# Kernel optimization log

Measured on AMD Instinct MI355X. Metric: run time of the kernel, lower is better.

The kernel has to match this reference:

```python
import jax, jax.numpy as jnp
import numpy as np

N_NODES = 20000
N_EDGES = 320000
D = 256          # out_channels (== in_channels here, so PyG zero-padding is a no-op)
NUM_LAYERS = 5


def setup_inputs() -> dict:
    key = jax.random.key(0)
    ks = jax.random.split(key, 8)
    x = jax.random.normal(ks[0], (N_NODES, D), dtype=jnp.float32)
    src = jax.random.randint(ks[1], (N_EDGES,), 0, N_NODES)
    dst = jax.random.randint(ks[2], (N_EDGES,), 0, N_NODES)
    edge_index = jnp.stack([src, dst]).astype(jnp.int64)
    edge_attr = jax.random.uniform(ks[3], (N_EDGES,), dtype=jnp.float32)
    s = 1.0 / np.sqrt(D)
    # per-layer message transform weights [L, D, D]
    weight = jax.random.uniform(ks[4], (NUM_LAYERS, D, D), minval=-s, maxval=s, dtype=jnp.float32)
    # GRUCell parameters (torch layout: [3*D, D] for W_ih/W_hh, [3*D] biases; gate order r, z, n)
    w_ih = jax.random.uniform(ks[5], (3 * D, D), minval=-s, maxval=s, dtype=jnp.float32)
    w_hh = jax.random.uniform(ks[6], (3 * D, D), minval=-s, maxval=s, dtype=jnp.float32)
    b = jax.random.uniform(ks[7], (2, 3 * D), minval=-s, maxval=s, dtype=jnp.float32)
    return {"x": x, "edge_index": edge_index, "edge_attr": edge_attr,
            "weight": weight, "w_ih": w_ih, "w_hh": w_hh,
            "b_ih": b[0], "b_hh": b[1]}


def gru_cell(m, h, w_ih, w_hh, b_ih, b_hh):
    gi = m @ w_ih.T + b_ih   # [N, 3D]
    gh = h @ w_hh.T + b_hh   # [N, 3D]
    i_r, i_z, i_n = jnp.split(gi, 3, axis=1)
    h_r, h_z, h_n = jnp.split(gh, 3, axis=1)
    r = jax.nn.sigmoid(i_r + h_r)
    z = jax.nn.sigmoid(i_z + h_z)
    n = jnp.tanh(i_n + r * h_n)
    return (1.0 - z) * n + z * h


def reference(x, edge_index, edge_attr, weight, w_ih, w_hh, b_ih, b_hh):
    src = edge_index[0]
    dst = edge_index[1]
    n_nodes = x.shape[0]
    h = x  # in_channels == out_channels, so no zero padding needed
    for i in range(weight.shape[0]):
        m = h @ weight[i]                                  # [N, D] transformed messages
        msgs = m[src] * edge_attr[:, None]                 # gather + edge weighting [E, D]
        agg = jax.ops.segment_sum(msgs, dst, num_segments=n_nodes)  # scatter-add [N, D]
        h = gru_cell(agg, h, w_ih, w_hh, b_ih, b_hh)
    return h
```

## Files before the change

### kernel.cpp

```cpp
#include <hip/hip_runtime.h>
#include <hip/hip_bf16.h>

#define NN 20000
#define NE 320000
#define DD 256

typedef __attribute__((ext_vector_type(8))) short bf16x8;
typedef __attribute__((ext_vector_type(4))) float f32x4;
typedef __attribute__((ext_vector_type(4))) int   int4v;
typedef __attribute__((ext_vector_type(4))) float float4v;

typedef __attribute__((address_space(1))) unsigned int gas_uint;
typedef __attribute__((address_space(3))) unsigned int las_uint;
static __device__ __forceinline__ void gload16(const void* g, void* l) {
    __builtin_amdgcn_global_load_lds((gas_uint*)g, (las_uint*)l, 16, 0, 0);
}

__device__ __forceinline__ unsigned short f2bf(float f) {
    union { float f; unsigned u; } v; v.f = f;
    unsigned r = v.u + 0x7fffu + ((v.u >> 16) & 1u);
    return (unsigned short)(r >> 16);
}
__device__ __forceinline__ float bf2f(unsigned short h) {
    union { unsigned u; float f; } v; v.u = ((unsigned)h) << 16;
    return v.f;
}
__device__ __forceinline__ float fast_sigmoid(float x) {
    return 1.f / (1.f + __expf(-x));
}
__device__ __forceinline__ float fast_tanh(float x) {
    x = fminf(fmaxf(x, -30.f), 30.f);
    float e = __expf(-2.f * x);
    return (1.f - e) / (1.f + e);
}

__global__ void prep_kernel(const float* __restrict__ x, unsigned short* __restrict__ hbfA,
                            const float* __restrict__ W, unsigned short* __restrict__ wnb,
                            const float* __restrict__ wih, unsigned short* __restrict__ wihb,
                            const float* __restrict__ whh, unsigned short* __restrict__ wc5,
                            const int* __restrict__ edst, int* __restrict__ deg) {
    const int b = blockIdx.x, t = threadIdx.x;
    if (b < 5000) {
        int i = (b * 256 + t) * 4;
        float4v v = *reinterpret_cast<const float4v*>(x + i);
        uint2 o;
        o.x = (unsigned)f2bf(v.x) | ((unsigned)f2bf(v.y) << 16);
        o.y = (unsigned)f2bf(v.z) | ((unsigned)f2bf(v.w) << 16);
        *reinterpret_cast<uint2*>(hbfA + i) = o;
    } else if (b < 5320) {
        int i = ((b - 5000) * 256 + t) * 4;
        float4v v = *reinterpret_cast<const float4v*>(W + i);
        uint2 o;
        o.x = (unsigned)f2bf(v.x) | ((unsigned)f2bf(v.y) << 16);
        o.y = (unsigned)f2bf(v.z) | ((unsigned)f2bf(v.w) << 16);
        *reinterpret_cast<uint2*>(wnb + i) = o;
    } else if (b < 5512) {
        int i = ((b - 5320) * 256 + t) * 4;
        float4v v = *reinterpret_cast<const float4v*>(wih + i);
        uint2 o;
        o.x = (unsigned)f2bf(v.x) | ((unsigned)f2bf(v.y) << 16);
        o.y = (unsigned)f2bf(v.z) | ((unsigned)f2bf(v.w) << 16);
        *reinterpret_cast<uint2*>(wihb + i) = o;
    } else if (b < 5704) {
        int id = (b - 5512) * 256 + t;
        int n3 = id >> 6, k0 = (id & 63) * 4;
        int g3 = (n3 >> 4) % 3;
        int d = (n3 / 48) * 16 + (n3 & 15);
        int gr = g3 * 256 + d;
        float4v v = *reinterpret_cast<const float4v*>(whh + gr * 256 + k0);
        uint2 o;
        o.x = (unsigned)f2bf(v.x) | ((unsigned)f2bf(v.y) << 16);
        o.y = (unsigned)f2bf(v.z) | ((unsigned)f2bf(v.w) << 16);
#pragma unroll
        for (int l = 0; l < 5; ++l)
            *reinterpret_cast<uint2*>(wc5 + ((size_t)(l * 2 + 1) * 768 + n3) * 256 + k0) = o;
    } else {
        int e = (b - 5704) * 256 + t;
        if (e < NE) atomicAdd(&deg[edst[e]], 1);
    }
}

__global__ __launch_bounds__(256) void pgemm_kernel(const unsigned short* __restrict__ A,
                                                    const unsigned short* __restrict__ Bt,
                                                    unsigned short* __restrict__ wc5) {
    __shared__ __align__(16) unsigned short As[128 * 64];
    __shared__ __align__(16) unsigned short Bs[64 * 64];
    const int t = threadIdx.x;
    const int lane = t & 63;
    const int w = t >> 6;
    const int wr = w >> 1, wc = w & 1;
    const int m0 = blockIdx.y * 128;
    const int n0 = blockIdx.x * 64;

    f32x4 acc[4][2];
    const f32x4 z4 = {0.f, 0.f, 0.f, 0.f};
    for (int i = 0; i < 4; ++i) for (int j = 0; j < 2; ++j) acc[i][j] = z4;

    for (int kt = 0; kt < 4; ++kt) {
        const int k0 = kt * 64;
#pragma unroll
        for (int rnd = 0; rnd < 4; ++rnd) {
            int cb = rnd * 256 + (w << 6);
            int c = cb + lane;
            int row = c >> 3, sl = c & 7;
            int gsl = sl ^ (row & 7);
            gload16(A + (size_t)(m0 + row) * 256 + k0 + gsl * 8, &As[cb * 8]);
        }
#pragma unroll
        for (int rnd = 0; rnd < 2; ++rnd) {
            int cb = rnd * 256 + (w << 6);
            int c = cb + lane;
            int row = c >> 3, sl = c & 7;
            int gsl = sl ^ (row & 7);
            gload16(Bt + (size_t)(n0 + row) * 256 + k0 + gsl * 8, &Bs[cb * 8]);
        }
        __syncthreads();
#pragma unroll
        for (int ks = 0; ks < 2; ++ks) {
            const int slot = ks * 4 + (lane >> 4);
            bf16x8 a[4], b[2];
#pragma unroll
            for (int mi = 0; mi < 4; ++mi) {
                int row = wr * 64 + mi * 16 + (lane & 15);
                a[mi] = *reinterpret_cast<const bf16x8*>(&As[row * 64 + ((slot ^ (row & 7)) << 3)]);
            }
#pragma unroll
            for (int ni = 0; ni < 2; ++ni) {
                int row = wc * 32 + ni * 16 + (lane & 15);
                b[ni] = *reinterpret_cast<const bf16x8*>(&Bs[row * 64 + ((slot ^ (row & 7)) << 3)]);
            }
#pragma unroll
            for (int mi = 0; mi < 4; ++mi)
#pragma unroll
                for (int ni = 0; ni < 2; ++ni)
                    acc[mi][ni] = __builtin_amdgcn_mfma_f32_16x16x32_bf16(a[mi], b[ni], acc[mi][ni], 0, 0, 0);
        }
        __syncthreads();
    }
#pragma unroll
    for (int mi = 0; mi < 4; ++mi)
#pragma unroll
        for (int ni = 0; ni < 2; ++ni)
#pragma unroll
            for (int r = 0; r < 4; ++r) {
                int grow = m0 + wr * 64 + mi * 16 + (lane >> 4) * 4 + r;
                int gcol = n0 + wc * 32 + ni * 16 + (lane & 15);
                int l = grow >> 8, k = grow & 255;
                int g3 = gcol >> 8, d = gcol & 255;
                int n3 = (d >> 4) * 48 + g3 * 16 + (d & 15);
                wc5[((size_t)(l * 2) * 768 + n3) * 256 + k] = f2bf(acc[mi][ni][r]);
            }
}


__global__ __launch_bounds__(1024) void scan_kernel(const int* __restrict__ deg, int* __restrict__ base) {
    __shared__ int part[1024];
    const int t = threadIdx.x;
    const int CH = 20;
    int start = t * CH;
    int s = 0;
    for (int i = 0; i < CH; ++i) { int idx = start + i; if (idx < NN) s += deg[idx]; }
    part[t] = s; __syncthreads();
    for (int off = 1; off < 1024; off <<= 1) {
        int v = (t >= off) ? part[t - off] : 0;
        __syncthreads();
        part[t] += v;
        __syncthreads();
    }
    int run = (t == 0) ? 0 : part[t - 1];
    for (int i = 0; i < CH; ++i) {
        int idx = start + i;
        if (idx < NN) { base[idx] = run; run += deg[idx]; }
    }
    if (t == 1023) base[NN] = run;
}

__global__ void fill_kernel(const int* __restrict__ src, const int* __restrict__ dst,
                            const float* __restrict__ attr, const int* __restrict__ base,
                            int* __restrict__ cursor, int* __restrict__ ssrc,
                            float* __restrict__ sattr) {
    int e = blockIdx.x * 256 + threadIdx.x;
    if (e >= NE) return;
    int d = dst[e];
    int pos = base[d] + atomicAdd(&cursor[d], 1);
    ssrc[pos] = src[e];
    sattr[pos] = attr[e];
}

__global__ __launch_bounds__(256) void gather_agg_kernel(const unsigned short* __restrict__ Hbf,
                                                         const int* __restrict__ base,
                                                         const int* __restrict__ ssrc,
                                                         const float* __restrict__ sattr,
                                                         unsigned short* __restrict__ AggBf) {
    int node = blockIdx.x * 4 + (threadIdx.x >> 6);
    if (node >= NN) return;
    int lane = threadIdx.x & 63;
    int q = lane >> 4;
    int ql = lane & 15;
    int b0 = base[node], b1 = base[node + 1];
    float ac[16];
#pragma unroll
    for (int j = 0; j < 16; ++j) ac[j] = 0.f;
    for (int p = b0 + q; p < b1; p += 4) {
        int s = ssrc[p];
        float a = sattr[p];
        const unsigned short* rowp = Hbf + (size_t)s * 256 + ql * 16;
        int4v v0 = *reinterpret_cast<const int4v*>(rowp);
        int4v v1 = *reinterpret_cast<const int4v*>(rowp + 8);
#pragma unroll
        for (int j = 0; j < 4; ++j) {
            unsigned u0 = (unsigned)v0[j];
            ac[2 * j]     += a * bf2f((unsigned short)(u0 & 0xffff));
            ac[2 * j + 1] += a * bf2f((unsigned short)(u0 >> 16));
            unsigned u1 = (unsigned)v1[j];
            ac[8 + 2 * j]     += a * bf2f((unsigned short)(u1 & 0xffff));
            ac[8 + 2 * j + 1] += a * bf2f((unsigned short)(u1 >> 16));
        }
    }
#pragma unroll
    for (int j = 0; j < 16; ++j) {
        ac[j] += __shfl_xor(ac[j], 16);
        ac[j] += __shfl_xor(ac[j], 32);
    }
    if (q == 0) {
        unsigned ou[8];
#pragma unroll
        for (int j = 0; j < 8; ++j)
            ou[j] = (unsigned)f2bf(ac[2 * j]) | ((unsigned)f2bf(ac[2 * j + 1]) << 16);
        unsigned short* op = AggBf + (size_t)node * 256 + ql * 16;
        *reinterpret_cast<int4v*>(op)     = *reinterpret_cast<int4v*>(&ou[0]);
        *reinterpret_cast<int4v*>(op + 8) = *reinterpret_cast<int4v*>(&ou[4]);
    }
}

__global__ __launch_bounds__(512) void gru4_kernel(const unsigned short* __restrict__ Abf,
                                                   const unsigned short* __restrict__ Hbf,
                                                   const unsigned short* __restrict__ Wc,
                                                   const float* __restrict__ b_ih,
                                                   const float* __restrict__ b_hh,
                                                   const float* __restrict__ x_f32,
                                                   float* __restrict__ h_out,
                                                   unsigned short* __restrict__ Hbf_out,
                                                   int first, int last) {
    __shared__ __align__(16) unsigned short As[128 * 64];
    __shared__ __align__(16) unsigned short Bs[96 * 64];
    const int t = threadIdx.x;
    const int lane = t & 63;
    const int w = t >> 6;
    const int wm = w >> 1, wn = w & 1;
    int b = blockIdx.x;
    int ww = (b & 7) * 158 + (b >> 3);
    const int mt = ww >> 3, dgp = ww & 7;
    const int m0 = mt * 128;

    f32x4 aR[2], aZ[2], aI[2], aH[2];
    const f32x4 z4 = {0.f, 0.f, 0.f, 0.f};
#pragma unroll
    for (int i = 0; i < 2; ++i) { aR[i] = z4; aZ[i] = z4; aI[i] = z4; aH[i] = z4; }

    auto do_half = [&](const unsigned short* __restrict__ aptr,
                       const unsigned short* __restrict__ wcb,
                       f32x4 (&aX)[2]) {
        for (int kq = 0; kq < 4; ++kq) {
            const int ka = kq * 64;
#pragma unroll
            for (int rnd = 0; rnd < 2; ++rnd) {
                int cb = rnd * 512 + (w << 6);
                int c = cb + lane;
                int row = c >> 3, sl = c & 7;
                int gsl = sl ^ (row & 7);
                gload16(aptr + (size_t)(m0 + row) * 256 + ka + gsl * 8, &As[cb * 8]);
            }
            {
                int cb = (w << 6);
                int c = cb + lane;
                int row = c >> 3, sl = c & 7;
                int gsl = sl ^ (row & 7);
                gload16(wcb + (size_t)(dgp * 96 + row) * 256 + ka + gsl * 8, &Bs[cb * 8]);
            }
            if (w < 4) {
                int cb = 512 + (w << 6);
                int c = cb + lane;
                int row = c >> 3, sl = c & 7;
                int gsl = sl ^ (row & 7);
                gload16(wcb + (size_t)(dgp * 96 + row) * 256 + ka + gsl * 8, &Bs[cb * 8]);
            }
            __syncthreads();
#pragma unroll
            for (int ks = 0; ks < 2; ++ks) {
                const int slot = ks * 4 + (lane >> 4);
                bf16x8 a[2], bfr[3];
#pragma unroll
                for (int mi = 0; mi < 2; ++mi) {
                    int row = wm * 32 + mi * 16 + (lane & 15);
                    a[mi] = *reinterpret_cast<const bf16x8*>(&As[row * 64 + ((slot ^ (row & 7)) << 3)]);
                }
#pragma unroll
                for (int g3 = 0; g3 < 3; ++g3) {
                    int row = wn * 48 + g3 * 16 + (lane & 15);
                    bfr[g3] = *reinterpret_cast<const bf16x8*>(&Bs[row * 64 + ((slot ^ (row & 7)) << 3)]);
                }
#pragma unroll
                for (int mi = 0; mi < 2; ++mi) {
                    aR[mi] = __builtin_amdgcn_mfma_f32_16x16x32_bf16(a[mi], bfr[0], aR[mi], 0, 0, 0);
                    aZ[mi] = __builtin_amdgcn_mfma_f32_16x16x32_bf16(a[mi], bfr[1], aZ[mi], 0, 0, 0);
                    aX[mi] = __builtin_amdgcn_mfma_f32_16x16x32_bf16(a[mi], bfr[2], aX[mi], 0, 0, 0);
                }
            }
            __syncthreads();
        }
    };

    do_half(Abf, Wc, aI);
    do_half(Hbf, Wc + 768 * 256, aH);

    const int d = (dgp * 2 + wn) * 16 + (lane & 15);
    const float bir = b_ih[d],        bhr = b_hh[d];
    const float biz = b_ih[256 + d],  bhz = b_hh[256 + d];
    const float bin_ = b_ih[512 + d], bhn = b_hh[512 + d];
#pragma unroll
    for (int mi = 0; mi < 2; ++mi)
#pragma unroll
        for (int r = 0; r < 4; ++r) {
            int grow = m0 + wm * 32 + mi * 16 + (lane >> 4) * 4 + r;
            if (grow >= NN) continue;
            size_t idx = (size_t)grow * 256 + d;
            float rr = fast_sigmoid(aR[mi][r] + bir + bhr);
            float zz = fast_sigmoid(aZ[mi][r] + biz + bhz);
            float nn = fast_tanh(aI[mi][r] + bin_ + rr * (aH[mi][r] + bhn));
            float hp = first ? x_f32[idx] : bf2f(Hbf[idx]);
            float hv = (1.f - zz) * nn + zz * hp;
            if (last) h_out[idx] = hv;
            Hbf_out[idx] = f2bf(hv);
        }
}


extern "C" void kernel_launch(void* const* d_in, const int* in_sizes, int n_in,
                              void* d_out, int out_size, void* d_ws, size_t ws_size,
                              hipStream_t stream) {
    const float* x     = (const float*)d_in[0];
    const int*   eidx  = (const int*)d_in[1];
    const float* eattr = (const float*)d_in[2];
    const float* W     = (const float*)d_in[3];
    const float* wih   = (const float*)d_in[4];
    const float* whh   = (const float*)d_in[5];
    const float* bih   = (const float*)d_in[6];
    const float* bhh   = (const float*)d_in[7];
    float* out = (float*)d_out;
    const int* esrc = eidx;
    const int* edst = eidx + NE;

    char* p = (char*)d_ws;
    auto alloc = [&](size_t bytes) -> char* {
        char* r = p; p += (bytes + 255) & ~(size_t)255; return r;
    };
    unsigned short* hbfA  = (unsigned short*)alloc((size_t)NN * DD * 2);
    unsigned short* hbfB  = (unsigned short*)alloc((size_t)NN * DD * 2);
    unsigned short* aggbf = (unsigned short*)alloc((size_t)NN * DD * 2);
    unsigned short* wnb   = (unsigned short*)alloc((size_t)5 * DD * DD * 2);
    unsigned short* wihb  = (unsigned short*)alloc((size_t)768 * DD * 2);
    unsigned short* wc5   = (unsigned short*)alloc((size_t)5 * 2 * 768 * 256 * 2);
    int*   degcur = (int*)alloc((size_t)2 * NN * 4);
    int*   deg    = degcur;
    int*   cursor = degcur + NN;
    int*   basep  = (int*)alloc((size_t)(NN + 1) * 4);
    int*   ssrc   = (int*)alloc((size_t)NE * 4);
    float* sattr  = (float*)alloc((size_t)NE * 4);
    alloc(262144);

    hipMemsetAsync(degcur, 0, (size_t)2 * NN * 4, stream);
    prep_kernel<<<6954, 256, 0, stream>>>(x, hbfA, W, wnb, wih, wihb, whh, wc5, edst, deg);
    pgemm_kernel<<<dim3(12, 10), 256, 0, stream>>>(wnb, wihb, wc5);
    scan_kernel<<<1, 1024, 0, stream>>>(deg, basep);
    fill_kernel<<<1250, 256, 0, stream>>>(esrc, edst, eattr, basep, cursor, ssrc, sattr);

    unsigned short* hb_cur = hbfA;
    unsigned short* hb_nxt = hbfB;
    for (int l = 0; l < 5; ++l) {
        gather_agg_kernel<<<5000, 256, 0, stream>>>(hb_cur, basep, ssrc, sattr, aggbf);
        gru4_kernel<<<1264, 512, 0, stream>>>(aggbf, hb_cur, wc5 + (size_t)l * 2 * 768 * 256,
                                              bih, bhh, x, out, hb_nxt,
                                              (l == 0) ? 1 : 0, (l == 4) ? 1 : 0);
        unsigned short* tmp = hb_cur; hb_cur = hb_nxt; hb_nxt = tmp;
    }
    (void)in_sizes; (void)n_in; (void)out_size; (void)ws_size;
}
```

Measured before the change: 343.8 us.

## Fuse all layers into one cooperative persistent kernel with grid syncs

Replaces the ten per-layer gather and GRU launches with a single cooperative persistent kernel that loops over layers and separates the aggregation and GRU phases with grid-wide syncs. It also drops the separate cursor array by atomically bumping the scan base directly in fill, then recovers each segment start as end minus degree. The goal is to remove launch gaps and tail effects between the many short kernels. The costs are a persistent grid capped by occupancy (launch bounds 512 threads, 8 blocks), grid-sync overhead, and host-side attribute and occupancy queries on every call.

```diff
diff --git a/kernel.cpp b/kernel.cpp
--- a/kernel.cpp
+++ b/kernel.cpp
@@ -1,5 +1,8 @@
 #include <hip/hip_runtime.h>
 #include <hip/hip_bf16.h>
+#include <hip/hip_cooperative_groups.h>
+
+namespace cg = cooperative_groups;
 
 #define NN 20000
 #define NE 320000
@@ -176,19 +179,19 @@
 }
 
 __global__ void fill_kernel(const int* __restrict__ src, const int* __restrict__ dst,
-                            const float* __restrict__ attr, const int* __restrict__ base,
-                            int* __restrict__ cursor, int* __restrict__ ssrc,
-                            float* __restrict__ sattr) {
+                            const float* __restrict__ attr, int* __restrict__ base,
+                            int* __restrict__ ssrc, float* __restrict__ sattr) {
     int e = blockIdx.x * 256 + threadIdx.x;
     if (e >= NE) return;
     int d = dst[e];
-    int pos = base[d] + atomicAdd(&cursor[d], 1);
+    int pos = atomicAdd(&base[d], 1);
     ssrc[pos] = src[e];
     sattr[pos] = attr[e];
 }
 
 __global__ __launch_bounds__(256) void gather_agg_kernel(const unsigned short* __restrict__ Hbf,
-                                                         const int* __restrict__ base,
+                                                         const int* __restrict__ basee,
+                                                         const int* __restrict__ deg,
                                                          const int* __restrict__ ssrc,
                                                          const float* __restrict__ sattr,
                                                          unsigned short* __restrict__ AggBf) {
@@ -197,7 +200,8 @@
     int lane = threadIdx.x & 63;
     int q = lane >> 4;
     int ql = lane & 15;
-    int b0 = base[node], b1 = base[node + 1];
+    int b1 = basee[node];
+    int b0 = b1 - deg[node];
     float ac[16];
 #pragma unroll
     for (int j = 0; j < 16; ++j) ac[j] = 0.f;
@@ -335,6 +339,160 @@
         }
 }
 
+__global__ __launch_bounds__(512, 8) void mega_kernel(
+        unsigned short* __restrict__ hbfA, unsigned short* __restrict__ hbfB,
+        unsigned short* __restrict__ aggbf, const unsigned short* __restrict__ wc5,
+        const int* __restrict__ basee, const int* __restrict__ deg,
+        const int* __restrict__ ssrc, const float* __restrict__ sattr,
+        const float* __restrict__ b_ih, const float* __restrict__ b_hh,
+        const float* __restrict__ x_f32, float* __restrict__ h_out) {
+    cg::grid_group grid = cg::this_grid();
+    __shared__ __align__(16) unsigned short As[128 * 64];
+    __shared__ __align__(16) unsigned short Bs[96 * 64];
+    const int t = threadIdx.x;
+    const int lane = t & 63;
+    const int w = t >> 6;
+    const int wm = w >> 1, wn = w & 1;
+    const int bid = blockIdx.x;
+    const int nblk = gridDim.x;
+
+    for (int l = 0; l < 5; ++l) {
+        const unsigned short* hcur = (l & 1) ? hbfB : hbfA;
+        unsigned short* hnxt = (l & 1) ? hbfA : hbfB;
+        const int first = (l == 0), last = (l == 4);
+
+        for (int node = bid * 8 + w; node < NN; node += nblk * 8) {
+            int q = lane >> 4;
+            int ql = lane & 15;
+            int b1 = basee[node];
+            int b0 = b1 - deg[node];
+            float ac[16];
+#pragma unroll
+            for (int j = 0; j < 16; ++j) ac[j] = 0.f;
+            for (int p = b0 + q; p < b1; p += 4) {
+                int s = ssrc[p];
+                float a = sattr[p];
+                const unsigned short* rowp = hcur + (size_t)s * 256 + ql * 16;
+                int4v v0 = *reinterpret_cast<const int4v*>(rowp);
+                int4v v1 = *reinterpret_cast<const int4v*>(rowp + 8);
+#pragma unroll
+                for (int j = 0; j < 4; ++j) {
+                    unsigned u0 = (unsigned)v0[j];
+                    ac[2 * j]     += a * bf2f((unsigned short)(u0 & 0xffff));
+                    ac[2 * j + 1] += a * bf2f((unsigned short)(u0 >> 16));
+                    unsigned u1 = (unsigned)v1[j];
+                    ac[8 + 2 * j]     += a * bf2f((unsigned short)(u1 & 0xffff));
+                    ac[8 + 2 * j + 1] += a * bf2f((unsigned short)(u1 >> 16));
+                }
+            }
+#pragma unroll
+            for (int j = 0; j < 16; ++j) {
+                ac[j] += __shfl_xor(ac[j], 16);
+                ac[j] += __shfl_xor(ac[j], 32);
+            }
+            if (q == 0) {
+                unsigned ou[8];
+#pragma unroll
+                for (int j = 0; j < 8; ++j)
+                    ou[j] = (unsigned)f2bf(ac[2 * j]) | ((unsigned)f2bf(ac[2 * j + 1]) << 16);
+                unsigned short* op = aggbf + (size_t)node * 256 + ql * 16;
+                *reinterpret_cast<int4v*>(op)     = *reinterpret_cast<int4v*>(&ou[0]);
+                *reinterpret_cast<int4v*>(op + 8) = *reinterpret_cast<int4v*>(&ou[4]);
+            }
+        }
+        grid.sync();
+
+        const unsigned short* Wc = wc5 + (size_t)l * 2 * 768 * 256;
+        for (int tile = bid; tile < 1264; tile += nblk) {
+            int ww = (tile & 7) * 158 + (tile >> 3);
+            const int mt = ww >> 3, dgp = ww & 7;
+            const int m0 = mt * 128;
+
+            f32x4 aR[2], aZ[2], aI[2], aH[2];
+            const f32x4 z4 = {0.f, 0.f, 0.f, 0.f};
+#pragma unroll
+            for (int i = 0; i < 2; ++i) { aR[i] = z4; aZ[i] = z4; aI[i] = z4; aH[i] = z4; }
+
+            auto do_half = [&](const unsigned short* __restrict__ aptr,
+                               const unsigned short* __restrict__ wcb,
+                               f32x4 (&aX)[2]) {
+                for (int kq = 0; kq < 4; ++kq) {
+                    const int ka = kq * 64;
+#pragma unroll
+                    for (int rnd = 0; rnd < 2; ++rnd) {
+                        int cb = rnd * 512 + (w << 6);
+                        int c = cb + lane;
+                        int row = c >> 3, sl = c & 7;
+                        int gsl = sl ^ (row & 7);
+                        gload16(aptr + (size_t)(m0 + row) * 256 + ka + gsl * 8, &As[cb * 8]);
+                    }
+                    {
+                        int cb = (w << 6);
+                        int c = cb + lane;
+                        int row = c >> 3, sl = c & 7;
+                        int gsl = sl ^ (row & 7);
+                        gload16(wcb + (size_t)(dgp * 96 + row) * 256 + ka + gsl * 8, &Bs[cb * 8]);
+                    }
+                    if (w < 4) {
+                        int cb = 512 + (w << 6);
+                        int c = cb + lane;
+                        int row = c >> 3, sl = c & 7;
+                        int gsl = sl ^ (row & 7);
+                        gload16(wcb + (size_t)(dgp * 96 + row) * 256 + ka + gsl * 8, &Bs[cb * 8]);
+                    }
+                    __syncthreads();
+#pragma unroll
+                    for (int ks = 0; ks < 2; ++ks) {
+                        const int slot = ks * 4 + (lane >> 4);
+                        bf16x8 a[2], bfr[3];
+#pragma unroll
+                        for (int mi = 0; mi < 2; ++mi) {
+                            int row = wm * 32 + mi * 16 + (lane & 15);
+                            a[mi] = *reinterpret_cast<const bf16x8*>(&As[row * 64 + ((slot ^ (row & 7)) << 3)]);
+                        }
+#pragma unroll
+                        for (int g3 = 0; g3 < 3; ++g3) {
+                            int row = wn * 48 + g3 * 16 + (lane & 15);
+                            bfr[g3] = *reinterpret_cast<const bf16x8*>(&Bs[row * 64 + ((slot ^ (row & 7)) << 3)]);
+                        }
+#pragma unroll
+                        for (int mi = 0; mi < 2; ++mi) {
+                            aR[mi] = __builtin_amdgcn_mfma_f32_16x16x32_bf16(a[mi], bfr[0], aR[mi], 0, 0, 0);
+                            aZ[mi] = __builtin_amdgcn_mfma_f32_16x16x32_bf16(a[mi], bfr[1], aZ[mi], 0, 0, 0);
+                            aX[mi] = __builtin_amdgcn_mfma_f32_16x16x32_bf16(a[mi], bfr[2], aX[mi], 0, 0, 0);
+                        }
+                    }
+                    __syncthreads();
+                }
+            };
+
+            do_half(aggbf, Wc, aI);
+            do_half(hcur, Wc + 768 * 256, aH);
+
+            const int d = (dgp * 2 + wn) * 16 + (lane & 15);
+            const float bir = b_ih[d],        bhr = b_hh[d];
+            const float biz = b_ih[256 + d],  bhz = b_hh[256 + d];
+            const float bin_ = b_ih[512 + d], bhn = b_hh[512 + d];
+#pragma unroll
+            for (int mi = 0; mi < 2; ++mi)
+#pragma unroll
+                for (int r = 0; r < 4; ++r) {
+                    int grow = m0 + wm * 32 + mi * 16 + (lane >> 4) * 4 + r;
+                    if (grow >= NN) continue;
+                    size_t idx = (size_t)grow * 256 + d;
+                    float rr = fast_sigmoid(aR[mi][r] + bir + bhr);
+                    float zz = fast_sigmoid(aZ[mi][r] + biz + bhz);
+                    float nn = fast_tanh(aI[mi][r] + bin_ + rr * (aH[mi][r] + bhn));
+                    float hp = first ? x_f32[idx] : bf2f(hcur[idx]);
+                    float hv = (1.f - zz) * nn + zz * hp;
+                    if (last) h_out[idx] = hv;
+                    hnxt[idx] = f2bf(hv);
+                }
+        }
+        grid.sync();
+    }
+}
+
 
 extern "C" void kernel_launch(void* const* d_in, const int* in_sizes, int n_in,
                               void* d_out, int out_size, void* d_ws, size_t ws_size,
@@ -361,28 +519,52 @@
     unsigned short* wnb   = (unsigned short*)alloc((size_t)5 * DD * DD * 2);
     unsigned short* wihb  = (unsigned short*)alloc((size_t)768 * DD * 2);
     unsigned short* wc5   = (unsigned short*)alloc((size_t)5 * 2 * 768 * 256 * 2);
-    int*   degcur = (int*)alloc((size_t)2 * NN * 4);
-    int*   deg    = degcur;
-    int*   cursor = degcur + NN;
+    int*   deg    = (int*)alloc((size_t)NN * 4);
     int*   basep  = (int*)alloc((size_t)(NN + 1) * 4);
     int*   ssrc   = (int*)alloc((size_t)NE * 4);
     float* sattr  = (float*)alloc((size_t)NE * 4);
     alloc(262144);
 
-    hipMemsetAsync(degcur, 0, (size_t)2 * NN * 4, stream);
+    hipMemsetAsync(deg, 0, (size_t)NN * 4, stream);
     prep_kernel<<<6954, 256, 0, stream>>>(x, hbfA, W, wnb, wih, wihb, whh, wc5, edst, deg);
     pgemm_kernel<<<dim3(12, 10), 256, 0, stream>>>(wnb, wihb, wc5);
     scan_kernel<<<1, 1024, 0, stream>>>(deg, basep);
-    fill_kernel<<<1250, 256, 0, stream>>>(esrc, edst, eattr, basep, cursor, ssrc, sattr);
-
-    unsigned short* hb_cur = hbfA;
-    unsigned short* hb_nxt = hbfB;
-    for (int l = 0; l < 5; ++l) {
-        gather_agg_kernel<<<5000, 256, 0, stream>>>(hb_cur, basep, ssrc, sattr, aggbf);
-        gru4_kernel<<<1264, 512, 0, stream>>>(aggbf, hb_cur, wc5 + (size_t)l * 2 * 768 * 256,
-                                              bih, bhh, x, out, hb_nxt,
-                                              (l == 0) ? 1 : 0, (l == 4) ? 1 : 0);
-        unsigned short* tmp = hb_cur; hb_cur = hb_nxt; hb_nxt = tmp;
+    fill_kernel<<<1250, 256, 0, stream>>>(esrc, edst, eattr, basep, ssrc, sattr);
+
+    bool coop_done = false;
+    int coop_attr = 0;
+    if (hipDeviceGetAttribute(&coop_attr, hipDeviceAttributeCooperativeLaunch, 0) == hipSuccess
+        && coop_attr) {
+        int maxb = 0;
+        if (hipOccupancyMaxActiveBlocksPerMultiprocessor(&maxb, mega_kernel, 512, 0) == hipSuccess
+            && maxb >= 4) {
+            hipDeviceProp_t prop;
+            if (hipGetDeviceProperties(&prop, 0) == hipSuccess) {
+                int grid = maxb * prop.multiProcessorCount;
+                if (grid > 1264) grid = 1264;
+                void* kargs[] = {
+                    (void*)&hbfA, (void*)&hbfB, (void*)&aggbf, (void*)&wc5,
+                    (void*)&basep, (void*)&deg, (void*)&ssrc, (void*)&sattr,
+                    (void*)&bih, (void*)&bhh, (void*)&x, (void*)&out
+                };
+                hipError_t e = hipLaunchCooperativeKernel((const void*)mega_kernel,
+                                                          dim3(grid), dim3(512),
+                                                          kargs, 0, stream);
+                coop_done = (e == hipSuccess);
+            }
+        }
+    }
+
+    if (!coop_done) {
+        unsigned short* hb_cur = hbfA;
+        unsigned short* hb_nxt = hbfB;
+        for (int l = 0; l < 5; ++l) {
+            gather_agg_kernel<<<5000, 256, 0, stream>>>(hb_cur, basep, deg, ssrc, sattr, aggbf);
+            gru4_kernel<<<1264, 512, 0, stream>>>(aggbf, hb_cur, wc5 + (size_t)l * 2 * 768 * 256,
+                                                  bih, bhh, x, out, hb_nxt,
+                                                  (l == 0) ? 1 : 0, (l == 4) ? 1 : 0);
+            unsigned short* tmp = hb_cur; hb_cur = hb_nxt; hb_nxt = tmp;
+        }
     }
     (void)in_sizes; (void)n_in; (void)out_size; (void)ws_size;
 }
```

New measurement: 344.1 us. No clear change (+0.1%).
